# Performance work log

Hardware: AMD Instinct MI355X
Metric: run time of the kernel (lower is better)

The kernel has to match this reference:

```python
import jax, jax.numpy as jnp
import numpy as np

L = 5      # n_levels
NH = 4     # num_heads
P = 4      # num_points
E = 256    # embed_dims
C = 256    # bev_dims
HB = 128
WB = 128
NQ = HB * WB
HD = E // NH
NL = 6     # num_layers
FF = 2 * E # ffn hidden


def setup_inputs() -> dict:
    key = jax.random.key(0)
    ks = jax.random.split(key, 12)
    s = 0.02
    def n(k, shape):
        return jax.random.normal(k, shape, jnp.float32) * s
    return dict(
        feat_bev=jax.random.normal(ks[0], (L, 1, C, HB, WB), jnp.float32),
        norm0_g=jnp.ones((L, C), jnp.float32), norm0_b=jnp.zeros((L, C), jnp.float32),
        in_w=n(ks[1], (C * L, E)), in_b=jnp.zeros((E,), jnp.float32),
        pos_row=n(ks[2], (HB, E // 2)), pos_col=n(ks[3], (WB, E // 2)),
        off_w=n(ks[4], (NL, E, NH * L * P * 2)), off_b=n(ks[5], (NL, NH * L * P * 2)),
        aw_w=n(ks[6], (NL, E, NH * L * P)), aw_b=jnp.zeros((NL, NH * L * P), jnp.float32),
        val_w=n(ks[7], (NL, C, E)), val_b=jnp.zeros((NL, E), jnp.float32),
        out_w=n(ks[8], (NL, E, E)), out_b=jnp.zeros((NL, E), jnp.float32),
        ln1_g=jnp.ones((NL, E), jnp.float32), ln1_b=jnp.zeros((NL, E), jnp.float32),
        ln2_g=jnp.ones((NL, E), jnp.float32), ln2_b=jnp.zeros((NL, E), jnp.float32),
        ffn_w1=n(ks[9], (NL, E, FF)), ffn_b1=jnp.zeros((NL, FF), jnp.float32),
        ffn_w2=n(ks[10], (NL, FF, E)), ffn_b2=jnp.zeros((NL, E), jnp.float32),
    )


def _ln(x, g, b):
    m = x.mean(-1, keepdims=True)
    v = ((x - m) ** 2).mean(-1, keepdims=True)
    return (x - m) * jax.lax.rsqrt(v + 1e-5) * g + b


def reference(feat_bev, norm0_g, norm0_b, in_w, in_b, pos_row, pos_col,
              off_w, off_b, aw_w, aw_b, val_w, val_b, out_w, out_b,
              ln1_g, ln1_b, ln2_g, ln2_b, ffn_w1, ffn_b1, ffn_w2, ffn_b2):
    Lv, bs, Cc, H, W = feat_bev.shape
    nq = H * W
    # per-level LN over channels (norm_layer0)
    f = feat_bev.transpose(0, 1, 3, 4, 2).reshape(Lv, bs, nq, Cc)
    f = _ln(f, norm0_g[:, None, None, :], norm0_b[:, None, None, :])  # [L, bs, nq, C]
    # input_proj on channel-concat of levels (level-major block rows of in_w)
    q = jnp.einsum('lbnc,lce->bne', f, in_w.reshape(Lv, Cc, E)) + in_b  # [bs, nq, E]
    # learned positional encoding: pos[h, w] = cat(col[w], row[h])
    pos = jnp.concatenate([
        jnp.broadcast_to(pos_col[None, :, :], (H, W, E // 2)),
        jnp.broadcast_to(pos_row[:, None, :], (H, W, E // 2))], -1).reshape(1, nq, E)
    # reference points (pixel centers, normalized)
    ys, xs = jnp.meshgrid(jnp.arange(H, dtype=jnp.float32) + 0.5,
                          jnp.arange(W, dtype=jnp.float32) + 0.5, indexing='ij')
    ref = jnp.stack([xs.ravel() / W, ys.ravel() / H], -1)  # [nq, 2] (x, y)
    norm = jnp.array([W, H], jnp.float32)
    b_ix = jnp.arange(bs)[:, None, None, None, None]
    h_ix = jnp.arange(NH)[None, None, :, None, None]
    l_ix = jnp.arange(Lv)[None, None, None, :, None]
    for i in range(NL):
        qp = q + pos
        off = (qp @ off_w[i] + off_b[i]).reshape(bs, nq, NH, Lv, P, 2)
        aw = jax.nn.softmax((qp @ aw_w[i] + aw_b[i]).reshape(bs, nq, NH, Lv * P), -1)
        aw = aw.reshape(bs, nq, NH, Lv, P)
        loc = ref[None, :, None, None, None, :] + off / norm
        x = loc[..., 0] * W - 0.5
        y = loc[..., 1] * H - 0.5
        x0 = jnp.floor(x); y0 = jnp.floor(y)
        fx = x - x0; fy = y - y0
        x0i = x0.astype(jnp.int32); y0i = y0.astype(jnp.int32)
        # per-layer value projection of normed multi-level features
        val = (jnp.einsum('lbnc,ce->blne', f, val_w[i]) + val_b[i]).reshape(bs, Lv, nq, NH, HD)
        acc = jnp.zeros((bs, nq, NH, HD), q.dtype)
        for dx, dy, wgt in ((0, 0, (1 - fx) * (1 - fy)), (1, 0, fx * (1 - fy)),
                            (0, 1, (1 - fx) * fy), (1, 1, fx * fy)):
            ix = x0i + dx; iy = y0i + dy
            valid = ((ix >= 0) & (ix < W) & (iy >= 0) & (iy < H)).astype(q.dtype)
            sidx = jnp.clip(iy, 0, H - 1) * W + jnp.clip(ix, 0, W - 1)
            g = val[b_ix, l_ix, sidx, h_ix]  # [bs, nq, NH, Lv, P, HD]
            acc = acc + jnp.einsum('bqhlp,bqhlpd->bqhd', wgt * valid * aw, g)
        q = q + (acc.reshape(bs, nq, NH * HD) @ out_w[i] + out_b[i])
        q = _ln(q, ln1_g[i], ln1_b[i])
        q = q + jax.nn.relu(q @ ffn_w1[i] + ffn_b1[i]) @ ffn_w2[i] + ffn_b2[i]
        q = _ln(q, ln2_g[i], ln2_b[i])
    return q.transpose(0, 2, 1).reshape(bs, E, H, W)
```

## Files before the change

kernel.cpp:

```cpp
#include <hip/hip_runtime.h>
#include <hip/hip_bf16.h>
#include <stdint.h>

static constexpr int kL  = 5;
static constexpr int kNH = 4;
static constexpr int kP  = 4;
static constexpr int kE  = 256;
static constexpr int kC  = 256;
static constexpr int kH  = 128;
static constexpr int kW  = 128;
static constexpr int kNQ = kH * kW;
static constexpr int kNL = 6;
static constexpr int kFF = 2 * kE;
static constexpr int kCOMB = 240;

typedef short bf16x8 __attribute__((ext_vector_type(8)));
typedef float f32x4 __attribute__((ext_vector_type(4)));

__device__ __forceinline__ short f2bf(float x) {
  union { float f; uint32_t u; } v; v.f = x;
  uint32_t r = v.u + 0x7fffu + ((v.u >> 16) & 1u);
  return (short)(r >> 16);
}
__device__ __forceinline__ uint32_t pack2(float a, float b) {
  return (uint32_t)(unsigned short)f2bf(a) | ((uint32_t)(unsigned short)f2bf(b) << 16);
}
__device__ __forceinline__ float bflo(uint32_t u) { return __uint_as_float(u << 16); }
__device__ __forceinline__ float bfhi(uint32_t u) { return __uint_as_float(u & 0xffff0000u); }
__device__ __forceinline__ float bf2f(unsigned short u) {
  return __uint_as_float((uint32_t)u << 16);
}

__device__ __forceinline__ void gl_lds16(const void* g, void* l) {
  __builtin_amdgcn_global_load_lds(
      (const __attribute__((address_space(1))) void*)g,
      (__attribute__((address_space(3))) void*)l, 16, 0, 0);
}

template <int BM, int MODE, int RB>
__global__ __launch_bounds__(512, MODE == 0 ? 4 : 2) void gemm2_kernel(
    const short* __restrict__ A, long sAb, int lda,
    const short* __restrict__ BT, int ldbt, int Kb, int nbatch,
    const float* __restrict__ bias,
    float* Cf, short* __restrict__ Cb, int ldc, int relu,
    const void* resid, const float* __restrict__ lng,
    const float* __restrict__ lnb, short* __restrict__ qp,
    const float* __restrict__ pos_row, const float* __restrict__ pos_col,
    const short* __restrict__ w2BT, const float* __restrict__ w2B,
    short* __restrict__ out2) {
  static_assert(BM == 64, "layout assumes BM=64");
  constexpr bool FUSED = (MODE == 3 || MODE == 4);
  constexpr int BK = 64;
  constexpr int KG = 2;
  constexpr int NW = 8;
  constexpr int WR = 2, WC = 4;
  constexpr int MT = BM / (16 * WR);
  constexpr int NT = 16 / WC;
  constexpr int AG = (BM / 16) * KG;
  constexpr int BG = 16 * KG;
  constexpr int ASZ = BM * BK;
  constexpr int BSZ = 256 * BK;
  __shared__ short smem[2 * ASZ + 2 * BSZ + (FUSED ? 64 * 280 : 0)];
  short* const Asm = smem;
  short* const Bsm = smem + 2 * ASZ;
  short* const qpS = smem + 2 * ASZ + 2 * BSZ;
  float2(*const lnpart)[WC] = (float2(*)[WC])smem;
  const int tid = threadIdx.x;
  const int wave = tid >> 6, lane = tid & 63;
  const int wy = wave >> 2, wx = wave & 3;
  const long row0 = (long)blockIdx.y * BM;
  const int col0 = blockIdx.x * 256;
  const int srow = lane >> 2;
  const int skof = ((lane & 3) ^ (srow & 3)) * 8;
  const int fr = lane & 15, fq = lane >> 4;
  const int ua = (fr * 4 + (fq ^ (fr & 3))) * 8;
  f32x4 acc[MT][NT] = {};
  const int KT = Kb >> 6;
  const int NTILES = nbatch * KT;

  auto stage_tile = [&](int buf, int bb, int kt) {
    const short* Ab = A + (long)bb * sAb + row0 * lda;
    const short* Bb = BT + (long)col0 * ldbt + (long)bb * Kb;
    int k0 = kt * BK;
#pragma unroll
    for (int t = wave; t < AG + BG; t += NW) {
      if (t < AG) {
        int rg = t >> 1, kg = t & 1;
        gl_lds16(Ab + (long)(rg * 16 + srow) * lda + k0 + kg * 32 + skof,
                 &Asm[buf * ASZ + t * 512]);
      } else {
        int u = t - AG;
        int rg = u >> 1, kg = u & 1;
        gl_lds16(Bb + (long)(rg * 16 + srow) * ldbt + k0 + kg * 32 + skof,
                 &Bsm[buf * BSZ + u * 512]);
      }
    }
  };

  int cur = 0;
  stage_tile(0, 0, 0);
  __syncthreads();
  int sb = 0, sk = 0;
  for (int idx = 0; idx < NTILES; ++idx) {
    if (idx + 1 < NTILES) {
      if (++sk == KT) { sk = 0; ++sb; }
      stage_tile(cur ^ 1, sb, sk);
    }
#pragma unroll
    for (int kk = 0; kk < KG; ++kk) {
      bf16x8 af[MT], bfv[NT];
#pragma unroll
      for (int t = 0; t < MT; ++t)
        af[t] = *(const bf16x8*)&Asm[cur * ASZ + ((wy * MT + t) * KG + kk) * 512 + ua];
#pragma unroll
      for (int t = 0; t < NT; ++t)
        bfv[t] = *(const bf16x8*)&Bsm[cur * BSZ + ((wx * 4 + t) * KG + kk) * 512 + ua];
#pragma unroll
      for (int mt = 0; mt < MT; ++mt)
#pragma unroll
        for (int nt = 0; nt < NT; ++nt)
          acc[mt][nt] = __builtin_amdgcn_mfma_f32_16x16x32_bf16(
              af[mt], bfv[nt], acc[mt][nt], 0, 0, 0);
    }
    __syncthreads();
    cur ^= 1;
  }

  const int colb = col0 + wx * 64 + fr;
  const long rowb = row0 + wy * 32 + fq * 4;

  if (MODE == 0) {
#pragma unroll
    for (int mt = 0; mt < MT; ++mt)
#pragma unroll
      for (int rr = 0; rr < 4; ++rr) {
        long row = rowb + mt * 16 + rr;
#pragma unroll
        for (int nt = 0; nt < NT; ++nt) {
          int col = colb + nt * 16;
          float v = acc[mt][nt][rr] + bias[col];
          if (relu) v = fmaxf(v, 0.f);
          if (Cf) Cf[row * ldc + col] = v;
          if (Cb) Cb[row * ldc + col] = f2bf(v);
        }
      }
  } else if (MODE == 2) {
#pragma unroll
    for (int mt = 0; mt < MT; ++mt)
#pragma unroll
      for (int rr = 0; rr < 4; ++rr) {
        long row = rowb + mt * 16 + rr;
        int wpos = (int)row & (kW - 1), hpos = (int)row >> 7;
#pragma unroll
        for (int nt = 0; nt < NT; ++nt) {
          int col = colb + nt * 16;
          float v = acc[mt][nt][rr] + bias[col];
          Cf[row * 256 + col] = v;
          float pv = (col < 128) ? pos_col[wpos * 128 + col]
                                 : pos_row[hpos * 128 + (col - 128)];
          qp[row * 256 + col] = f2bf(v + pv);
        }
      }
  } else {
    const float* residf = (const float*)resid;
    const unsigned short* residb = (const unsigned short*)resid;
#pragma unroll
    for (int mt = 0; mt < MT; ++mt)
#pragma unroll
      for (int rr = 0; rr < 4; ++rr) {
        long row = rowb + mt * 16 + rr;
        float s = 0.f, s2 = 0.f;
#pragma unroll
        for (int nt = 0; nt < NT; ++nt) {
          int col = colb + nt * 16;
          float rv = RB ? bf2f(residb[row * 256 + col])
                        : residf[row * 256 + col];
          float v = acc[mt][nt][rr] + bias[col] + rv;
          acc[mt][nt][rr] = v;
          s += v; s2 += v * v;
        }
#pragma unroll
        for (int o = 8; o > 0; o >>= 1) {
          s += __shfl_xor(s, o);
          s2 += __shfl_xor(s2, o);
        }
        if (fr == 0) {
          int rl = wy * 32 + mt * 16 + fq * 4 + rr;
          lnpart[rl][wx] = make_float2(s, s2);
        }
      }
    __syncthreads();
#pragma unroll
    for (int mt = 0; mt < MT; ++mt)
#pragma unroll
      for (int rr = 0; rr < 4; ++rr) {
        int rl = wy * 32 + mt * 16 + fq * 4 + rr;
        long row = rowb + mt * 16 + rr;
        float s = 0.f, s2 = 0.f;
#pragma unroll
        for (int c = 0; c < WC; ++c) {
          s += lnpart[rl][c].x; s2 += lnpart[rl][c].y;
        }
        float m = s * (1.f / 256);
        float var = s2 * (1.f / 256) - m * m;
        float rs = rsqrtf(var + 1e-5f);
        int wpos = (int)row & (kW - 1), hpos = (int)row >> 7;
#pragma unroll
        for (int nt = 0; nt < NT; ++nt) {
          int col = colb + nt * 16;
          float y = (acc[mt][nt][rr] - m) * rs * lng[col] + lnb[col];
          if (Cf) Cf[row * 256 + col] = y;
          if (MODE != 3 && Cb) Cb[row * 256 + col] = f2bf(y);
          if (MODE == 1 && qp) {
            float pv = (col < 128) ? pos_col[wpos * 128 + col]
                                   : pos_row[hpos * 128 + (col - 128)];
            qp[row * 256 + col] = f2bf(y + pv);
          }
          if (MODE == 3) {
            float pv = (col < 128) ? pos_col[wpos * 128 + col]
                                   : pos_row[hpos * 128 + (col - 128)];
            qpS[rl * 280 + col] = f2bf(y + pv);
          }
          if (MODE == 4) qpS[rl * 280 + col] = f2bf(y);
        }
      }
    if constexpr (FUSED) {
      __syncthreads();
      constexpr int ld2 = (MODE == 4) ? 512 : 256;
      constexpr int MT2 = BM / 16;
      constexpr int NT2 = (MODE == 4) ? 8 : 4;
      auto stageW = [&](int buf, int t2) {
        int hf = t2 >> 2;
        int k0 = (t2 & 3) * BK;
#pragma unroll
        for (int u = wave; u < BG; u += NW) {
          int rg = u >> 1, kg = u & 1;
          gl_lds16(w2BT + (long)(hf * 256 + rg * 16 + srow) * 256 + k0 +
                       kg * 32 + skof,
                   &Bsm[buf * BSZ + u * 512]);
        }
      };
      f32x4 acc2[MT2][NT] = {};
      stageW(cur, 0);
      __syncthreads();
      for (int t2 = 0; t2 < NT2; ++t2) {
        if (t2 + 1 < NT2) stageW(cur ^ 1, t2 + 1);
        int k0 = (t2 & 3) * BK;
#pragma unroll
        for (int kk = 0; kk < KG; ++kk) {
          bf16x8 av[MT2], bv[NT];
#pragma unroll
          for (int mt = 0; mt < MT2; ++mt)
            av[mt] = *(const bf16x8*)&qpS[(mt * 16 + fr) * 280 + k0 +
                                          kk * 32 + fq * 8];
#pragma unroll
          for (int t = 0; t < NT; ++t)
            bv[t] = *(const bf16x8*)&Bsm[cur * BSZ + ((wx * 4 + t) * KG + kk) *
                                             512 + ua];
#pragma unroll
          for (int mt = 0; mt < MT2; ++mt)
#pragma unroll
            for (int t = 0; t < NT; ++t)
              acc2[mt][t] = __builtin_amdgcn_mfma_f32_16x16x32_bf16(
                  av[mt], bv[t], acc2[mt][t], 0, 0, 0);
        }
        if ((t2 & 3) == 3) {
          int hf = t2 >> 2;
#pragma unroll
          for (int mt = 0; mt < MT2; ++mt)
#pragma unroll
            for (int rr = 0; rr < 4; ++rr) {
              long row = row0 + mt * 16 + fq * 4 + rr;
#pragma unroll
              for (int nt = 0; nt < NT; ++nt) {
                int oc = hf * 256 + wx * 64 + nt * 16 + fr;
                float v = acc2[mt][nt][rr] + w2B[oc];
                if (MODE == 4) v = fmaxf(v, 0.f);
                out2[row * ld2 + oc] = f2bf(v);
              }
            }
#pragma unroll
          for (int mt = 0; mt < MT2; ++mt)
#pragma unroll
            for (int t = 0; t < NT; ++t)
              acc2[mt][t] = f32x4{0.f, 0.f, 0.f, 0.f};
        }
        __syncthreads();
        cur ^= 1;
      }
    }
  }
}

__global__ __launch_bounds__(256) void wt_convert_kernel(
    const float* __restrict__ in, short* __restrict__ out, int K, int N) {
  long idx = (long)blockIdx.x * 256 + threadIdx.x;
  int z = blockIdx.y;
  int n = (int)(idx / K);
  int k = (int)(idx - (long)n * K);
  out[(long)z * N * K + idx] = f2bf(in[(long)z * K * N + (long)k * N + n]);
}

__global__ __launch_bounds__(256) void comb_convert_kernel(
    const float* __restrict__ off_w, const float* __restrict__ aw_w,
    const float* __restrict__ off_b, const float* __restrict__ aw_b,
    short* __restrict__ combT, float* __restrict__ comb_bias) {
  int idx = blockIdx.x * 256 + threadIdx.x;
  int z = blockIdx.y;
  int n = idx >> 8, k = idx & 255;
  float v = 0.f;
  if (n < 160) v = off_w[((long)z * 256 + k) * 160 + n];
  else if (n < kCOMB) v = aw_w[((long)z * 256 + k) * 80 + (n - 160)];
  combT[(long)z * 65536 + idx] = f2bf(v);
  if (k == 0)
    comb_bias[z * 256 + n] =
        (n < 160) ? off_b[z * 160 + n]
                  : (n < kCOMB ? aw_b[z * 80 + (n - 160)] : 0.f);
}

__global__ __launch_bounds__(256) void ln_stats_kernel(
    const float* __restrict__ feat, float* __restrict__ mean_out,
    float* __restrict__ rstd_out) {
  int i = blockIdx.x * 256 + threadIdx.x;
  int l = i >> 14;
  int n = i & (kNQ - 1);
  const float* base = feat + (long)l * kC * kNQ + n;
  float s = 0.f, s2 = 0.f;
  for (int c = 0; c < kC; ++c) {
    float v = base[(long)c * kNQ];
    s += v; s2 += v * v;
  }
  float m = s * (1.f / kC);
  float var = s2 * (1.f / kC) - m * m;
  mean_out[i] = m;
  rstd_out[i] = rsqrtf(var + 1e-5f);
}

__global__ __launch_bounds__(256) void ln_apply_kernel(
    const float* __restrict__ feat, const float* __restrict__ mean_in,
    const float* __restrict__ rstd_in, const float* __restrict__ g,
    const float* __restrict__ b, short* __restrict__ f) {
  __shared__ float tile[32][33];
  int l  = blockIdx.z;
  int cb = blockIdx.x * 32, nb = blockIdx.y * 32;
  int tx = threadIdx.x & 31;
  int ty = threadIdx.x >> 5;
#pragma unroll
  for (int j = 0; j < 4; ++j) {
    int c = ty + j * 8;
    tile[c][tx] = feat[((long)(l * kC + cb + c)) * kNQ + nb + tx];
  }
  __syncthreads();
#pragma unroll
  for (int j = 0; j < 4; ++j) {
    int nl = ty + j * 8;
    int n  = nb + nl;
    float m  = mean_in[l * kNQ + n];
    float rs = rstd_in[l * kNQ + n];
    int c = cb + tx;
    float v = (tile[tx][nl] - m) * rs * g[l * kC + c] + b[l * kC + c];
    f[((long)l * kNQ + n) * kC + c] = f2bf(v);
  }
}

__global__ __launch_bounds__(256) void sample_kernel(
    const unsigned short* __restrict__ comb, const short* __restrict__ val,
    short* __restrict__ accb) {
  __shared__ float2 ic[4][2][4][85];
  int wv = threadIdx.x >> 6;
  int lane = threadIdx.x & 63;
  int half = lane >> 5;
  int hl = lane & 31;
  int n = blockIdx.x * 8 + wv * 2 + half;
  int wq = n & (kW - 1);
  int hq = n >> 7;
  const unsigned short* cb = comb + (long)n * 256;
#pragma unroll
  for (int h = 0; h < 4; ++h) {
    float raw = (hl < 20) ? bf2f(cb[160 + h * 20 + hl]) : -1e30f;
    float mx = raw;
#pragma unroll
    for (int o = 16; o > 0; o >>= 1) mx = fmaxf(mx, __shfl_xor(mx, o));
    float ev = (hl < 20) ? __expf(raw - mx) : 0.f;
    float se = ev;
#pragma unroll
    for (int o = 16; o > 0; o >>= 1) se += __shfl_xor(se, o);
    if (hl < 20) {
      float awv = ev / se;
      int l = hl >> 2;
      float ox = bf2f(cb[h * 40 + hl * 2 + 0]);
      float oy = bf2f(cb[h * 40 + hl * 2 + 1]);
      float x = (float)wq + ox;
      float y = (float)hq + oy;
      float x0f = floorf(x), y0f = floorf(y);
      float fx = x - x0f, fy = y - y0f;
      int x0 = (int)x0f, y0 = (int)y0f;
#pragma unroll
      for (int c = 0; c < 4; ++c) {
        int dx = c & 1, dy = c >> 1;
        int ix = x0 + dx, iy = y0 + dy;
        float wgt = (dx ? fx : 1.f - fx) * (dy ? fy : 1.f - fy);
        bool valid = (ix >= 0 && ix < kW && iy >= 0 && iy < kH);
        int cix = min(max(ix, 0), kW - 1);
        int ciy = min(max(iy, 0), kH - 1);
        int sidx = ciy * kW + cix;
        int byteoff = (l * kNQ + sidx) * (kE * 2);
        float coef = valid ? awv * wgt : 0.f;
        ic[wv][half][h][hl * 4 + c] = make_float2(__int_as_float(byteoff), coef);
      }
    }
  }
  __syncthreads();
  int h2 = (lane >> 3) & 3;
  int ch8 = (lane & 7) * 8;
  const char* vb = (const char*)val + (h2 * 64 + ch8) * 2;
  const float2* icp = &ic[wv][half][h2][0];
  float a0 = 0.f, a1 = 0.f, a2 = 0.f, a3 = 0.f;
  float a4 = 0.f, a5 = 0.f, a6 = 0.f, a7 = 0.f;
#pragma unroll 4
  for (int j = 0; j < 80; ++j) {
    float2 oc = icp[j];
    int off = __float_as_int(oc.x);
    uint4 u = *(const uint4*)(vb + off);
    float cf = oc.y;
    a0 += cf * bflo(u.x); a1 += cf * bfhi(u.x);
    a2 += cf * bflo(u.y); a3 += cf * bfhi(u.y);
    a4 += cf * bflo(u.z); a5 += cf * bfhi(u.z);
    a6 += cf * bflo(u.w); a7 += cf * bfhi(u.w);
  }
  uint4 o;
  o.x = pack2(a0, a1); o.y = pack2(a2, a3);
  o.z = pack2(a4, a5); o.w = pack2(a6, a7);
  *(uint4*)(accb + (long)n * kE + h2 * 64 + ch8) = o;
}

__global__ __launch_bounds__(256) void transpose_kernel(
    const float* __restrict__ q, float* __restrict__ out) {
  __shared__ float t[32][33];
  int eb = blockIdx.x * 32, nb = blockIdx.y * 32;
  int tx = threadIdx.x & 31, ty = threadIdx.x >> 5;
#pragma unroll
  for (int j = 0; j < 4; ++j)
    t[ty + j * 8][tx] = q[(long)(nb + ty + j * 8) * kE + eb + tx];
  __syncthreads();
#pragma unroll
  for (int j = 0; j < 4; ++j)
    out[(long)(eb + ty + j * 8) * kNQ + nb + tx] = t[tx][ty + j * 8];
}

extern "C" void kernel_launch(void* const* d_in, const int* in_sizes, int n_in,
                              void* d_out, int out_size, void* d_ws,
                              size_t ws_size, hipStream_t stream) {
  const float* feat    = (const float*)d_in[0];
  const float* norm0_g = (const float*)d_in[1];
  const float* norm0_b = (const float*)d_in[2];
  const float* in_w    = (const float*)d_in[3];
  const float* in_b    = (const float*)d_in[4];
  const float* pos_row = (const float*)d_in[5];
  const float* pos_col = (const float*)d_in[6];
  const float* off_w   = (const float*)d_in[7];
  const float* off_b   = (const float*)d_in[8];
  const float* aw_w    = (const float*)d_in[9];
  const float* aw_b    = (const float*)d_in[10];
  const float* val_w   = (const float*)d_in[11];
  const float* val_b   = (const float*)d_in[12];
  const float* out_w   = (const float*)d_in[13];
  const float* out_b   = (const float*)d_in[14];
  const float* ln1_g   = (const float*)d_in[15];
  const float* ln1_b   = (const float*)d_in[16];
  const float* ln2_g   = (const float*)d_in[17];
  const float* ln2_b   = (const float*)d_in[18];
  const float* ffn_w1  = (const float*)d_in[19];
  const float* ffn_b1  = (const float*)d_in[20];
  const float* ffn_w2  = (const float*)d_in[21];
  const float* ffn_b2  = (const float*)d_in[22];

  char* p = (char*)d_ws;
  auto alloc = [&](size_t bytes) -> char* {
    char* r = p;
    p += (bytes + 255) & ~(size_t)255;
    return r;
  };
  short* f_bf    = (short*)alloc((size_t)kL * kNQ * kC * 2);
  short* val_bf  = (short*)alloc((size_t)kL * kNQ * kE * 2);
  float* q       = (float*)alloc((size_t)kNQ * kE * 4);
  short* qbf     = (short*)alloc((size_t)kNQ * kE * 2);
  short* qp_bf   = (short*)alloc((size_t)kNQ * kE * 2);
  short* accb    = (short*)alloc((size_t)kNQ * kE * 2);
  short* hid_bf  = (short*)alloc((size_t)kNQ * kFF * 2);
  short* comb_bf = (short*)alloc((size_t)kNQ * 256 * 2);
  float* comb_b  = (float*)alloc((size_t)kNL * 256 * 4);
  float* meanb   = (float*)alloc((size_t)kL * kNQ * 4);
  float* rstdb   = (float*)alloc((size_t)kL * kNQ * 4);
  short* inT     = (short*)alloc((size_t)256 * 1280 * 2);
  short* valT    = (short*)alloc((size_t)kNL * 256 * 256 * 2);
  short* outT    = (short*)alloc((size_t)kNL * 256 * 256 * 2);
  short* ffn1T   = (short*)alloc((size_t)kNL * 512 * 256 * 2);
  short* ffn2T   = (short*)alloc((size_t)kNL * 256 * 512 * 2);
  short* combT   = (short*)alloc((size_t)kNL * 256 * 256 * 2);

  wt_convert_kernel<<<dim3(1280, 1), 256, 0, stream>>>(in_w, inT, 1280, 256);
  wt_convert_kernel<<<dim3(256, kNL), 256, 0, stream>>>(val_w, valT, 256, 256);
  wt_convert_kernel<<<dim3(256, kNL), 256, 0, stream>>>(out_w, outT, 256, 256);
  wt_convert_kernel<<<dim3(512, kNL), 256, 0, stream>>>(ffn_w1, ffn1T, 256, 512);
  wt_convert_kernel<<<dim3(512, kNL), 256, 0, stream>>>(ffn_w2, ffn2T, 512, 256);
  comb_convert_kernel<<<dim3(256, kNL), 256, 0, stream>>>(off_w, aw_w, off_b,
                                                          aw_b, combT, comb_b);

  ln_stats_kernel<<<kL * kNQ / 256, 256, 0, stream>>>(feat, meanb, rstdb);
  ln_apply_kernel<<<dim3(kC / 32, kNQ / 32, kL), 256, 0, stream>>>(
      feat, meanb, rstdb, norm0_g, norm0_b, f_bf);

  gemm2_kernel<64, 2, 0><<<dim3(1, kNQ / 64), 512, 0, stream>>>(
      f_bf, (long)kNQ * kC, kC, inT, 1280, 256, kL, in_b,
      q, nullptr, 256, 0, nullptr, nullptr, nullptr, qp_bf, pos_row, pos_col,
      nullptr, nullptr, nullptr);
  gemm2_kernel<64, 0, 0><<<dim3(1, kNQ / 64), 512, 0, stream>>>(
      qp_bf, 0, kE, combT, 256, 256, 1, comb_b,
      nullptr, comb_bf, 256, 0, nullptr, nullptr, nullptr, nullptr,
      nullptr, nullptr, nullptr, nullptr, nullptr);

  for (int i = 0; i < kNL; ++i) {
    const short* valT_i  = valT + (long)i * 256 * 256;
    const short* outT_i  = outT + (long)i * 256 * 256;
    const short* f1T_i   = ffn1T + (long)i * 512 * 256;
    const short* f2T_i   = ffn2T + (long)i * 256 * 512;

    gemm2_kernel<64, 0, 0><<<dim3(1, kL * kNQ / 64), 512, 0, stream>>>(
        f_bf, 0, kC, valT_i, 256, 256, 1, val_b + (long)i * kE,
        nullptr, val_bf, kE, 0, nullptr, nullptr, nullptr, nullptr,
        nullptr, nullptr, nullptr, nullptr, nullptr);
    sample_kernel<<<kNQ / 8, 256, 0, stream>>>((const unsigned short*)comb_bf,
                                               val_bf, accb);
    gemm2_kernel<64, 4, 0><<<dim3(1, kNQ / 64), 512, 0, stream>>>(
        accb, 0, kE, outT_i, 256, 256, 1, out_b + (long)i * kE,
        nullptr, qbf, 256, 0, q, ln1_g + (long)i * kE, ln1_b + (long)i * kE,
        nullptr, nullptr, nullptr, f1T_i, ffn_b1 + (long)i * kFF, hid_bf);
    if (i + 1 < kNL) {
      gemm2_kernel<64, 3, 1><<<dim3(1, kNQ / 64), 512, 0, stream>>>(
          hid_bf, 0, kFF, f2T_i, 512, 512, 1, ffn_b2 + (long)i * kE,
          q, nullptr, 256, 0, qbf, ln2_g + (long)i * kE,
          ln2_b + (long)i * kE, nullptr, pos_row, pos_col,
          combT + (long)(i + 1) * 256 * 256, comb_b + (i + 1) * 256, comb_bf);
    } else {
      gemm2_kernel<64, 1, 1><<<dim3(1, kNQ / 64), 512, 0, stream>>>(
          hid_bf, 0, kFF, f2T_i, 512, 512, 1, ffn_b2 + (long)i * kE,
          q, nullptr, 256, 0, qbf, ln2_g + (long)i * kE,
          ln2_b + (long)i * kE, nullptr, nullptr, nullptr,
          nullptr, nullptr, nullptr);
    }
  }

  transpose_kernel<<<dim3(kE / 32, kNQ / 32), 256, 0, stream>>>(q,
                                                                (float*)d_out);
}
```

Before: 984.3 us.

## Batch value projections, fuse LN stats/apply, merge weight converts and input-proj+comb GEMM

The six per-layer value-projection GEMMs are replaced by two launches that each compute three layers at once (grid.x=3, output slab offset per z), with the sample kernel reading the slab for layer i%3. The two LayerNorm kernels are fused into a single one that computes stats and applies them from a 256x32 LDS tile. The six weight-conversion launches become one, and the input-projection GEMM now fuses the offset/attention-weight GEMM through LDS instead of writing qp_bf. This cuts launches and intermediate traffic and widens the value GEMMs, but triples the val_bf buffer and adds LDS pressure to the LN kernel.

```diff
diff --git a/kernel.cpp b/kernel.cpp
--- a/kernel.cpp
+++ b/kernel.cpp
@@ -42,20 +42,19 @@
     const short* __restrict__ A, long sAb, int lda,
     const short* __restrict__ BT, int ldbt, int Kb, int nbatch,
     const float* __restrict__ bias,
-    float* Cf, short* __restrict__ Cb, int ldc, int relu,
+    float* Cf, short* __restrict__ Cb, int ldc, int relu, long zouts,
     const void* resid, const float* __restrict__ lng,
     const float* __restrict__ lnb, short* __restrict__ qp,
     const float* __restrict__ pos_row, const float* __restrict__ pos_col,
     const short* __restrict__ w2BT, const float* __restrict__ w2B,
     short* __restrict__ out2) {
   static_assert(BM == 64, "layout assumes BM=64");
-  constexpr bool FUSED = (MODE == 3 || MODE == 4);
+  constexpr bool FUSED = (MODE == 3 || MODE == 4 || MODE == 5);
   constexpr int BK = 64;
   constexpr int KG = 2;
   constexpr int NW = 8;
-  constexpr int WR = 2, WC = 4;
-  constexpr int MT = BM / (16 * WR);
-  constexpr int NT = 16 / WC;
+  constexpr int MT = 2;
+  constexpr int NT = 4;
   constexpr int AG = (BM / 16) * KG;
   constexpr int BG = 16 * KG;
   constexpr int ASZ = BM * BK;
@@ -64,7 +63,7 @@
   short* const Asm = smem;
   short* const Bsm = smem + 2 * ASZ;
   short* const qpS = smem + 2 * ASZ + 2 * BSZ;
-  float2(*const lnpart)[WC] = (float2(*)[WC])smem;
+  float2(*const lnpart)[4] = (float2(*)[4])smem;
   const int tid = threadIdx.x;
   const int wave = tid >> 6, lane = tid & 63;
   const int wy = wave >> 2, wx = wave & 3;
@@ -130,6 +129,7 @@
   const long rowb = row0 + wy * 32 + fq * 4;
 
   if (MODE == 0) {
+    const long zoff = (long)blockIdx.x * zouts;
 #pragma unroll
     for (int mt = 0; mt < MT; ++mt)
 #pragma unroll
@@ -141,15 +141,16 @@
           float v = acc[mt][nt][rr] + bias[col];
           if (relu) v = fmaxf(v, 0.f);
           if (Cf) Cf[row * ldc + col] = v;
-          if (Cb) Cb[row * ldc + col] = f2bf(v);
-        }
-      }
-  } else if (MODE == 2) {
+          if (Cb) Cb[zoff + row * ldc + col] = f2bf(v);
+        }
+      }
+  } else if (MODE == 5) {
 #pragma unroll
     for (int mt = 0; mt < MT; ++mt)
 #pragma unroll
       for (int rr = 0; rr < 4; ++rr) {
         long row = rowb + mt * 16 + rr;
+        int rl = wy * 32 + mt * 16 + fq * 4 + rr;
         int wpos = (int)row & (kW - 1), hpos = (int)row >> 7;
 #pragma unroll
         for (int nt = 0; nt < NT; ++nt) {
@@ -158,7 +159,7 @@
           Cf[row * 256 + col] = v;
           float pv = (col < 128) ? pos_col[wpos * 128 + col]
                                  : pos_row[hpos * 128 + (col - 128)];
-          qp[row * 256 + col] = f2bf(v + pv);
+          qpS[rl * 280 + col] = f2bf(v + pv);
         }
       }
   } else {
@@ -198,7 +199,7 @@
         long row = rowb + mt * 16 + rr;
         float s = 0.f, s2 = 0.f;
 #pragma unroll
-        for (int c = 0; c < WC; ++c) {
+        for (int c = 0; c < 4; ++c) {
           s += lnpart[rl][c].x; s2 += lnpart[rl][c].y;
         }
         float m = s * (1.f / 256);
@@ -224,142 +225,173 @@
           if (MODE == 4) qpS[rl * 280 + col] = f2bf(y);
         }
       }
-    if constexpr (FUSED) {
+  }
+  if constexpr (FUSED) {
+    __syncthreads();
+    constexpr int ld2 = (MODE == 4) ? 512 : 256;
+    constexpr int MT2 = BM / 16;
+    constexpr int NT2 = (MODE == 4) ? 8 : 4;
+    auto stageW = [&](int buf, int t2) {
+      int hf = t2 >> 2;
+      int k0 = (t2 & 3) * BK;
+#pragma unroll
+      for (int u = wave; u < BG; u += NW) {
+        int rg = u >> 1, kg = u & 1;
+        gl_lds16(w2BT + (long)(hf * 256 + rg * 16 + srow) * 256 + k0 +
+                     kg * 32 + skof,
+                 &Bsm[buf * BSZ + u * 512]);
+      }
+    };
+    f32x4 acc2[MT2][NT] = {};
+    stageW(cur, 0);
+    __syncthreads();
+    for (int t2 = 0; t2 < NT2; ++t2) {
+      if (t2 + 1 < NT2) stageW(cur ^ 1, t2 + 1);
+      int k0 = (t2 & 3) * BK;
+#pragma unroll
+      for (int kk = 0; kk < KG; ++kk) {
+        bf16x8 av[MT2], bv[NT];
+#pragma unroll
+        for (int mt = 0; mt < MT2; ++mt)
+          av[mt] = *(const bf16x8*)&qpS[(mt * 16 + fr) * 280 + k0 +
+                                        kk * 32 + fq * 8];
+#pragma unroll
+        for (int t = 0; t < NT; ++t)
+          bv[t] = *(const bf16x8*)&Bsm[cur * BSZ + ((wx * 4 + t) * KG + kk) *
+                                           512 + ua];
+#pragma unroll
+        for (int mt = 0; mt < MT2; ++mt)
+#pragma unroll
+          for (int t = 0; t < NT; ++t)
+            acc2[mt][t] = __builtin_amdgcn_mfma_f32_16x16x32_bf16(
+                av[mt], bv[t], acc2[mt][t], 0, 0, 0);
+      }
+      if ((t2 & 3) == 3) {
+        int hf = t2 >> 2;
+#pragma unroll
+        for (int mt = 0; mt < MT2; ++mt)
+#pragma unroll
+          for (int rr = 0; rr < 4; ++rr) {
+            long row = row0 + mt * 16 + fq * 4 + rr;
+#pragma unroll
+            for (int nt = 0; nt < NT; ++nt) {
+              int oc = hf * 256 + wx * 64 + nt * 16 + fr;
+              float v = acc2[mt][nt][rr] + w2B[oc];
+              if (MODE == 4) v = fmaxf(v, 0.f);
+              out2[row * ld2 + oc] = f2bf(v);
+            }
+          }
+#pragma unroll
+        for (int mt = 0; mt < MT2; ++mt)
+#pragma unroll
+          for (int t = 0; t < NT; ++t)
+            acc2[mt][t] = f32x4{0.f, 0.f, 0.f, 0.f};
+      }
       __syncthreads();
-      constexpr int ld2 = (MODE == 4) ? 512 : 256;
-      constexpr int MT2 = BM / 16;
-      constexpr int NT2 = (MODE == 4) ? 8 : 4;
-      auto stageW = [&](int buf, int t2) {
-        int hf = t2 >> 2;
-        int k0 = (t2 & 3) * BK;
-#pragma unroll
-        for (int u = wave; u < BG; u += NW) {
-          int rg = u >> 1, kg = u & 1;
-          gl_lds16(w2BT + (long)(hf * 256 + rg * 16 + srow) * 256 + k0 +
-                       kg * 32 + skof,
-                   &Bsm[buf * BSZ + u * 512]);
-        }
-      };
-      f32x4 acc2[MT2][NT] = {};
-      stageW(cur, 0);
-      __syncthreads();
-      for (int t2 = 0; t2 < NT2; ++t2) {
-        if (t2 + 1 < NT2) stageW(cur ^ 1, t2 + 1);
-        int k0 = (t2 & 3) * BK;
-#pragma unroll
-        for (int kk = 0; kk < KG; ++kk) {
-          bf16x8 av[MT2], bv[NT];
-#pragma unroll
-          for (int mt = 0; mt < MT2; ++mt)
-            av[mt] = *(const bf16x8*)&qpS[(mt * 16 + fr) * 280 + k0 +
-                                          kk * 32 + fq * 8];
-#pragma unroll
-          for (int t = 0; t < NT; ++t)
-            bv[t] = *(const bf16x8*)&Bsm[cur * BSZ + ((wx * 4 + t) * KG + kk) *
-                                             512 + ua];
-#pragma unroll
-          for (int mt = 0; mt < MT2; ++mt)
-#pragma unroll
-            for (int t = 0; t < NT; ++t)
-              acc2[mt][t] = __builtin_amdgcn_mfma_f32_16x16x32_bf16(
-                  av[mt], bv[t], acc2[mt][t], 0, 0, 0);
-        }
-        if ((t2 & 3) == 3) {
-          int hf = t2 >> 2;
-#pragma unroll
-          for (int mt = 0; mt < MT2; ++mt)
-#pragma unroll
-            for (int rr = 0; rr < 4; ++rr) {
-              long row = row0 + mt * 16 + fq * 4 + rr;
-#pragma unroll
-              for (int nt = 0; nt < NT; ++nt) {
-                int oc = hf * 256 + wx * 64 + nt * 16 + fr;
-                float v = acc2[mt][nt][rr] + w2B[oc];
-                if (MODE == 4) v = fmaxf(v, 0.f);
-                out2[row * ld2 + oc] = f2bf(v);
-              }
-            }
-#pragma unroll
-          for (int mt = 0; mt < MT2; ++mt)
-#pragma unroll
-            for (int t = 0; t < NT; ++t)
-              acc2[mt][t] = f32x4{0.f, 0.f, 0.f, 0.f};
-        }
-        __syncthreads();
-        cur ^= 1;
-      }
-    }
-  }
-}
-
-__global__ __launch_bounds__(256) void wt_convert_kernel(
-    const float* __restrict__ in, short* __restrict__ out, int K, int N) {
-  long idx = (long)blockIdx.x * 256 + threadIdx.x;
-  int z = blockIdx.y;
-  int n = (int)(idx / K);
-  int k = (int)(idx - (long)n * K);
-  out[(long)z * N * K + idx] = f2bf(in[(long)z * K * N + (long)k * N + n]);
-}
-
-__global__ __launch_bounds__(256) void comb_convert_kernel(
-    const float* __restrict__ off_w, const float* __restrict__ aw_w,
-    const float* __restrict__ off_b, const float* __restrict__ aw_b,
+      cur ^= 1;
+    }
+  }
+}
+
+__global__ __launch_bounds__(256) void convert_all_kernel(
+    const float* __restrict__ in_w, const float* __restrict__ val_w,
+    const float* __restrict__ out_w, const float* __restrict__ ffn_w1,
+    const float* __restrict__ ffn_w2, const float* __restrict__ off_w,
+    const float* __restrict__ aw_w, const float* __restrict__ off_b,
+    const float* __restrict__ aw_b,
+    short* __restrict__ inT, short* __restrict__ valT, short* __restrict__ outT,
+    short* __restrict__ ffn1T, short* __restrict__ ffn2T,
     short* __restrict__ combT, float* __restrict__ comb_bias) {
-  int idx = blockIdx.x * 256 + threadIdx.x;
-  int z = blockIdx.y;
-  int n = idx >> 8, k = idx & 255;
-  float v = 0.f;
-  if (n < 160) v = off_w[((long)z * 256 + k) * 160 + n];
-  else if (n < kCOMB) v = aw_w[((long)z * 256 + k) * 80 + (n - 160)];
-  combT[(long)z * 65536 + idx] = f2bf(v);
-  if (k == 0)
-    comb_bias[z * 256 + n] =
-        (n < 160) ? off_b[z * 160 + n]
-                  : (n < kCOMB ? aw_b[z * 80 + (n - 160)] : 0.f);
-}
-
-__global__ __launch_bounds__(256) void ln_stats_kernel(
-    const float* __restrict__ feat, float* __restrict__ mean_out,
-    float* __restrict__ rstd_out) {
-  int i = blockIdx.x * 256 + threadIdx.x;
-  int l = i >> 14;
-  int n = i & (kNQ - 1);
-  const float* base = feat + (long)l * kC * kNQ + n;
-  float s = 0.f, s2 = 0.f;
-  for (int c = 0; c < kC; ++c) {
-    float v = base[(long)c * kNQ];
-    s += v; s2 += v * v;
-  }
-  float m = s * (1.f / kC);
-  float var = s2 * (1.f / kC) - m * m;
-  mean_out[i] = m;
-  rstd_out[i] = rsqrtf(var + 1e-5f);
-}
-
-__global__ __launch_bounds__(256) void ln_apply_kernel(
-    const float* __restrict__ feat, const float* __restrict__ mean_in,
-    const float* __restrict__ rstd_in, const float* __restrict__ g,
+  long e = (long)blockIdx.x * 256 + threadIdx.x;
+  if (e < 327680) {
+    int idx = (int)e;
+    int n = idx / 1280, k = idx - n * 1280;
+    inT[idx] = f2bf(in_w[(long)k * 256 + n]);
+    return;
+  }
+  e -= 327680;
+  if (e < 393216) {
+    int z = (int)(e >> 16), idx = (int)e & 65535;
+    int n = idx >> 8, k = idx & 255;
+    valT[e] = f2bf(val_w[((long)z * 256 + k) * 256 + n]);
+    return;
+  }
+  e -= 393216;
+  if (e < 393216) {
+    int z = (int)(e >> 16), idx = (int)e & 65535;
+    int n = idx >> 8, k = idx & 255;
+    outT[e] = f2bf(out_w[((long)z * 256 + k) * 256 + n]);
+    return;
+  }
+  e -= 393216;
+  if (e < 786432) {
+    int z = (int)(e / 131072);
+    int idx = (int)(e - (long)z * 131072);
+    int n = idx >> 8, k = idx & 255;
+    ffn1T[e] = f2bf(ffn_w1[((long)z * 256 + k) * 512 + n]);
+    return;
+  }
+  e -= 786432;
+  if (e < 786432) {
+    int z = (int)(e / 131072);
+    int idx = (int)(e - (long)z * 131072);
+    int n = idx >> 9, k = idx & 511;
+    ffn2T[e] = f2bf(ffn_w2[((long)z * 512 + k) * 256 + n]);
+    return;
+  }
+  e -= 786432;
+  {
+    int z = (int)(e >> 16), idx = (int)e & 65535;
+    int n = idx >> 8, k = idx & 255;
+    float v = 0.f;
+    if (n < 160) v = off_w[((long)z * 256 + k) * 160 + n];
+    else if (n < kCOMB) v = aw_w[((long)z * 256 + k) * 80 + (n - 160)];
+    combT[e] = f2bf(v);
+    if (k == 0)
+      comb_bias[z * 256 + n] =
+          (n < 160) ? off_b[z * 160 + n]
+                    : (n < kCOMB ? aw_b[z * 80 + (n - 160)] : 0.f);
+  }
+}
+
+__global__ __launch_bounds__(256) void ln_fused_kernel(
+    const float* __restrict__ feat, const float* __restrict__ g,
     const float* __restrict__ b, short* __restrict__ f) {
-  __shared__ float tile[32][33];
-  int l  = blockIdx.z;
-  int cb = blockIdx.x * 32, nb = blockIdx.y * 32;
+  __shared__ float tile[256][33];
+  __shared__ float2 part[8][32];
+  __shared__ float mS[32], rsS[32];
+  int l = blockIdx.y;
+  int n0 = blockIdx.x * 32;
   int tx = threadIdx.x & 31;
   int ty = threadIdx.x >> 5;
-#pragma unroll
-  for (int j = 0; j < 4; ++j) {
-    int c = ty + j * 8;
-    tile[c][tx] = feat[((long)(l * kC + cb + c)) * kNQ + nb + tx];
-  }
+  float s = 0.f, s2 = 0.f;
+#pragma unroll 8
+  for (int j = 0; j < 32; ++j) {
+    int c = ty * 32 + j;
+    float v = feat[((long)(l * kC + c)) * kNQ + n0 + tx];
+    tile[c][tx] = v;
+    s += v; s2 += v * v;
+  }
+  part[ty][tx] = make_float2(s, s2);
   __syncthreads();
-#pragma unroll
-  for (int j = 0; j < 4; ++j) {
-    int nl = ty + j * 8;
-    int n  = nb + nl;
-    float m  = mean_in[l * kNQ + n];
-    float rs = rstd_in[l * kNQ + n];
-    int c = cb + tx;
-    float v = (tile[tx][nl] - m) * rs * g[l * kC + c] + b[l * kC + c];
-    f[((long)l * kNQ + n) * kC + c] = f2bf(v);
+  if (ty == 0) {
+    float ss = 0.f, ss2 = 0.f;
+#pragma unroll
+    for (int j = 0; j < 8; ++j) {
+      ss += part[j][tx].x; ss2 += part[j][tx].y;
+    }
+    float m = ss * (1.f / kC);
+    float var = ss2 * (1.f / kC) - m * m;
+    mS[tx] = m;
+    rsS[tx] = rsqrtf(var + 1e-5f);
+  }
+  __syncthreads();
+  int c = threadIdx.x;
+  float gv = g[l * kC + c], bv = b[l * kC + c];
+#pragma unroll 8
+  for (int r = 0; r < 32; ++r) {
+    float v = (tile[c][r] - mS[r]) * rsS[r] * gv + bv;
+    f[((long)l * kNQ + n0 + r) * kC + c] = f2bf(v);
   }
 }
 
@@ -481,17 +513,15 @@
     p += (bytes + 255) & ~(size_t)255;
     return r;
   };
+  const size_t valSlab = (size_t)kL * kNQ * kE;
   short* f_bf    = (short*)alloc((size_t)kL * kNQ * kC * 2);
-  short* val_bf  = (short*)alloc((size_t)kL * kNQ * kE * 2);
+  short* val_bf  = (short*)alloc(3 * valSlab * 2);
   float* q       = (float*)alloc((size_t)kNQ * kE * 4);
   short* qbf     = (short*)alloc((size_t)kNQ * kE * 2);
-  short* qp_bf   = (short*)alloc((size_t)kNQ * kE * 2);
   short* accb    = (short*)alloc((size_t)kNQ * kE * 2);
   short* hid_bf  = (short*)alloc((size_t)kNQ * kFF * 2);
   short* comb_bf = (short*)alloc((size_t)kNQ * 256 * 2);
   float* comb_b  = (float*)alloc((size_t)kNL * 256 * 4);
-  float* meanb   = (float*)alloc((size_t)kL * kNQ * 4);
-  float* rstdb   = (float*)alloc((size_t)kL * kNQ * 4);
   short* inT     = (short*)alloc((size_t)256 * 1280 * 2);
   short* valT    = (short*)alloc((size_t)kNL * 256 * 256 * 2);
   short* outT    = (short*)alloc((size_t)kNL * 256 * 256 * 2);
@@ -499,53 +529,52 @@
   short* ffn2T   = (short*)alloc((size_t)kNL * 256 * 512 * 2);
   short* combT   = (short*)alloc((size_t)kNL * 256 * 256 * 2);
 
-  wt_convert_kernel<<<dim3(1280, 1), 256, 0, stream>>>(in_w, inT, 1280, 256);
-  wt_convert_kernel<<<dim3(256, kNL), 256, 0, stream>>>(val_w, valT, 256, 256);
-  wt_convert_kernel<<<dim3(256, kNL), 256, 0, stream>>>(out_w, outT, 256, 256);
-  wt_convert_kernel<<<dim3(512, kNL), 256, 0, stream>>>(ffn_w1, ffn1T, 256, 512);
-  wt_convert_kernel<<<dim3(512, kNL), 256, 0, stream>>>(ffn_w2, ffn2T, 512, 256);
-  comb_convert_kernel<<<dim3(256, kNL), 256, 0, stream>>>(off_w, aw_w, off_b,
-                                                          aw_b, combT, comb_b);
-
-  ln_stats_kernel<<<kL * kNQ / 256, 256, 0, stream>>>(feat, meanb, rstdb);
-  ln_apply_kernel<<<dim3(kC / 32, kNQ / 32, kL), 256, 0, stream>>>(
-      feat, meanb, rstdb, norm0_g, norm0_b, f_bf);
-
-  gemm2_kernel<64, 2, 0><<<dim3(1, kNQ / 64), 512, 0, stream>>>(
+  convert_all_kernel<<<12032, 256, 0, stream>>>(
+      in_w, val_w, out_w, ffn_w1, ffn_w2, off_w, aw_w, off_b, aw_b,
+      inT, valT, outT, ffn1T, ffn2T, combT, comb_b);
+
+  ln_fused_kernel<<<dim3(kNQ / 32, kL), 256, 0, stream>>>(feat, norm0_g,
+                                                          norm0_b, f_bf);
+
+  const long zouts = (long)kL * kNQ * 256 - 256;
+  gemm2_kernel<64, 0, 0><<<dim3(3, kL * kNQ / 64), 512, 0, stream>>>(
+      f_bf, 0, kC, valT, 256, 256, 1, val_b,
+      nullptr, val_bf, kE, 0, zouts, nullptr, nullptr, nullptr, nullptr,
+      nullptr, nullptr, nullptr, nullptr, nullptr);
+
+  gemm2_kernel<64, 5, 0><<<dim3(1, kNQ / 64), 512, 0, stream>>>(
       f_bf, (long)kNQ * kC, kC, inT, 1280, 256, kL, in_b,
-      q, nullptr, 256, 0, nullptr, nullptr, nullptr, qp_bf, pos_row, pos_col,
-      nullptr, nullptr, nullptr);
-  gemm2_kernel<64, 0, 0><<<dim3(1, kNQ / 64), 512, 0, stream>>>(
-      qp_bf, 0, kE, combT, 256, 256, 1, comb_b,
-      nullptr, comb_bf, 256, 0, nullptr, nullptr, nullptr, nullptr,
-      nullptr, nullptr, nullptr, nullptr, nullptr);
+      q, nullptr, 256, 0, 0, nullptr, nullptr, nullptr, nullptr,
+      pos_row, pos_col, combT, comb_b, comb_bf);
 
   for (int i = 0; i < kNL; ++i) {
-    const short* valT_i  = valT + (long)i * 256 * 256;
     const short* outT_i  = outT + (long)i * 256 * 256;
     const short* f1T_i   = ffn1T + (long)i * 512 * 256;
     const short* f2T_i   = ffn2T + (long)i * 256 * 512;
 
-    gemm2_kernel<64, 0, 0><<<dim3(1, kL * kNQ / 64), 512, 0, stream>>>(
-        f_bf, 0, kC, valT_i, 256, 256, 1, val_b + (long)i * kE,
-        nullptr, val_bf, kE, 0, nullptr, nullptr, nullptr, nullptr,
-        nullptr, nullptr, nullptr, nullptr, nullptr);
-    sample_kernel<<<kNQ / 8, 256, 0, stream>>>((const unsigned short*)comb_bf,
-                                               val_bf, accb);
+    sample_kernel<<<kNQ / 8, 256, 0, stream>>>(
+        (const unsigned short*)comb_bf, val_bf + (long)(i % 3) * valSlab,
+        accb);
+    if (i == 2) {
+      gemm2_kernel<64, 0, 0><<<dim3(3, kL * kNQ / 64), 512, 0, stream>>>(
+          f_bf, 0, kC, valT + 3 * 256 * 256, 256, 256, 1, val_b + 3 * kE,
+          nullptr, val_bf, kE, 0, zouts, nullptr, nullptr, nullptr, nullptr,
+          nullptr, nullptr, nullptr, nullptr, nullptr);
+    }
     gemm2_kernel<64, 4, 0><<<dim3(1, kNQ / 64), 512, 0, stream>>>(
         accb, 0, kE, outT_i, 256, 256, 1, out_b + (long)i * kE,
-        nullptr, qbf, 256, 0, q, ln1_g + (long)i * kE, ln1_b + (long)i * kE,
+        nullptr, qbf, 256, 0, 0, q, ln1_g + (long)i * kE, ln1_b + (long)i * kE,
         nullptr, nullptr, nullptr, f1T_i, ffn_b1 + (long)i * kFF, hid_bf);
     if (i + 1 < kNL) {
       gemm2_kernel<64, 3, 1><<<dim3(1, kNQ / 64), 512, 0, stream>>>(
           hid_bf, 0, kFF, f2T_i, 512, 512, 1, ffn_b2 + (long)i * kE,
-          q, nullptr, 256, 0, qbf, ln2_g + (long)i * kE,
+          q, nullptr, 256, 0, 0, qbf, ln2_g + (long)i * kE,
           ln2_b + (long)i * kE, nullptr, pos_row, pos_col,
           combT + (long)(i + 1) * 256 * 256, comb_b + (i + 1) * 256, comb_bf);
     } else {
       gemm2_kernel<64, 1, 1><<<dim3(1, kNQ / 64), 512, 0, stream>>>(
           hid_bf, 0, kFF, f2T_i, 512, 512, 1, ffn_b2 + (long)i * kE,
-          q, nullptr, 256, 0, qbf, ln2_g + (long)i * kE,
+          q, nullptr, 256, 0, 0, qbf, ln2_g + (long)i * kE,
           ln2_b + (long)i * kE, nullptr, nullptr, nullptr,
           nullptr, nullptr, nullptr);
     }
```

After: 959.1 us. 1.03x faster.
